# Optimization experiments

Hardware: AMD Instinct MI355X
Metric: run time of the kernel (lower is better)

## Reference

```python
import jax, jax.numpy as jnp
import numpy as np

N_NODES = 10000


def _add_self_loops(edge_index, n):
    loops = jnp.arange(n, dtype=edge_index.dtype)
    row = jnp.concatenate([edge_index[0], loops])
    col = jnp.concatenate([edge_index[1], loops])
    return row, col


def _gcn_norm(row, col, n):
    # symmetric normalization: deg^-1/2[row] * deg^-1/2[col], deg counted on col
    deg = jax.ops.segment_sum(jnp.ones_like(col, dtype=jnp.float32), col, num_segments=n)
    dis = jnp.where(deg > 0, jax.lax.rsqrt(jnp.maximum(deg, 1.0)), 0.0)
    return dis[row] * dis[col]


def _gcn_conv(x, W, b, row, col, norm, n):
    h = x @ W                      # [N, out]
    m = h[row] * norm[:, None]     # [E+N, out] gathered, normalized messages
    out = jax.ops.segment_sum(m, col, num_segments=n)
    return out + b


def setup_inputs() -> dict:
    key = jax.random.key(0)
    ks = jax.random.split(key, 10)
    N, E, Cin, Cout = N_NODES, 160000, 256, 512
    x = jax.random.normal(ks[0], (N, Cin), dtype=jnp.float32)
    edge_index = jax.random.randint(ks[1], (2, E), 0, N, dtype=jnp.int64)
    s = 1.0 / np.sqrt(Cin)
    s2 = 1.0 / np.sqrt(Cout)
    return {
        "x": x,
        "edge_index": edge_index,
        "W1": jax.random.normal(ks[2], (Cin, Cout), dtype=jnp.float32) * s,
        "b1": jnp.zeros((Cout,), dtype=jnp.float32),
        "W2": jax.random.normal(ks[3], (Cout, Cout), dtype=jnp.float32) * s2,
        "b2": jnp.zeros((Cout,), dtype=jnp.float32),
        "W3": jax.random.normal(ks[4], (Cout, Cout), dtype=jnp.float32) * s2,
        "b3": jnp.zeros((Cout,), dtype=jnp.float32),
        "W4": jax.random.normal(ks[5], (Cout, Cout), dtype=jnp.float32) * s2,
        "b4": jnp.zeros((Cout,), dtype=jnp.float32),
    }


def reference(x, edge_index, W1, b1, W2, b2, W3, b3, W4, b4):
    n = x.shape[0]
    row, col = _add_self_loops(edge_index, n)
    norm = _gcn_norm(row, col, n)
    h = jax.nn.relu(_gcn_conv(x, W1, b1, row, col, norm, n))
    h = jax.nn.relu(_gcn_conv(h, W2, b2, row, col, norm, n))
    h = jax.nn.relu(_gcn_conv(h, W3, b3, row, col, norm, n))
    h = _gcn_conv(h, W4, b4, row, col, norm, n)
    return h.reshape(-1, 5, h.shape[-1])  # [N/5, 5, 512]
```

## Files before the change

kernel.cpp:

```cpp
#include <hip/hip_runtime.h>
#include <hip/hip_bf16.h>

#define N_NODES 10000
#define N_EDGES 160000

typedef __hip_bfloat16 bf16;
typedef unsigned short u16;
typedef float f32x4 __attribute__((ext_vector_type(4)));
typedef short s16x8 __attribute__((ext_vector_type(8)));
typedef unsigned short us8 __attribute__((ext_vector_type(8)));
typedef unsigned short us4 __attribute__((ext_vector_type(4)));

static __device__ __forceinline__ float b2f(u16 u) {
    unsigned v = (unsigned)u << 16;
    return __uint_as_float(v);
}
static __device__ __forceinline__ u16 f2b(float f) {
    bf16 b = __float2bfloat16(f);
    return *reinterpret_cast<u16*>(&b);
}

#define GLDS(gp, lp)                                                         \
    __builtin_amdgcn_global_load_lds(                                        \
        (const __attribute__((address_space(1))) void*)(const void*)(gp),    \
        (__attribute__((address_space(3))) void*)(lp), 16, 0, 0)


__global__ void k_prep0(const int* __restrict__ ei,
                        int* __restrict__ row, int* __restrict__ col,
                        int* __restrict__ deg) {
    bool is64 = true;
#pragma unroll
    for (int i = 0; i < 8; ++i) is64 = is64 && (ei[2 * i + 1] == 0);
    int t = blockIdx.x * 256 + threadIdx.x;
    if (t < N_NODES) deg[t] = 0;
    if (t < N_EDGES) {
        if (is64) {
            row[t] = ei[2 * t];
            col[t] = ei[2 * (N_EDGES + t)];
        } else {
            row[t] = ei[t];
            col[t] = ei[N_EDGES + t];
        }
    }
}

__global__ void k_count(const int* __restrict__ col, int* deg) {
    int e = blockIdx.x * 256 + threadIdx.x;
    if (e < N_EDGES) atomicAdd(&deg[col[e]], 1);
}

__global__ void k_scan_all(const int* __restrict__ deg, float* __restrict__ dis,
                           int* __restrict__ off, int* __restrict__ cur) {
    __shared__ int sums[256];
    int t = threadIdx.x;
    const int seg = (N_NODES + 255) >> 8;
    int lo = t * seg, hi = lo + seg;
    if (lo > N_NODES) lo = N_NODES;
    if (hi > N_NODES) hi = N_NODES;
    int s = 0;
    for (int i = lo; i < hi; ++i) {
        dis[i] = rsqrtf((float)deg[i] + 1.0f);
        s += deg[i];
    }
    sums[t] = s;
    __syncthreads();
    for (int d = 1; d < 256; d <<= 1) {
        int v = (t >= d) ? sums[t - d] : 0;
        __syncthreads();
        sums[t] += v;
        __syncthreads();
    }
    int run = sums[t] - s;
    for (int i = lo; i < hi; ++i) {
        off[i] = run;
        cur[i] = run;
        run += deg[i];
    }
    if (t == 255) off[N_NODES] = sums[255];
}

__global__ void k_fill(const int* __restrict__ row, const int* __restrict__ col,
                       const float* __restrict__ dis, int* cur,
                       int* __restrict__ crow, float* __restrict__ cnorm) {
    int e = blockIdx.x * 256 + threadIdx.x;
    if (e < N_EDGES) {
        int r = row[e], c = col[e];
        int p = atomicAdd(&cur[c], 1);
        crow[p] = r;
        cnorm[p] = dis[r] * dis[c];
    }
}


__global__ void k_convx(const float* __restrict__ x, u16* __restrict__ xb) {
    int i = blockIdx.x * 256 + threadIdx.x;
    float4 v = *(const float4*)(x + (size_t)i * 4);
    us4 st;
    st[0] = f2b(v.x); st[1] = f2b(v.y); st[2] = f2b(v.z); st[3] = f2b(v.w);
    *(us4*)(xb + (size_t)i * 4) = st;
}


__global__ void k_transpose(const float* __restrict__ W1, const float* __restrict__ W2,
                            const float* __restrict__ W3, const float* __restrict__ W4,
                            u16* __restrict__ T1, u16* __restrict__ T2,
                            u16* __restrict__ T3, u16* __restrict__ T4) {
    __shared__ u16 tile[32][33];
    int z = blockIdx.z;
    const float* W = (z == 0) ? W1 : (z == 1) ? W2 : (z == 2) ? W3 : W4;
    u16* WT        = (z == 0) ? T1 : (z == 1) ? T2 : (z == 2) ? T3 : T4;
    int K = (z == 0) ? 256 : 512;
    int k0 = blockIdx.y * 32;
    if (k0 >= K) return;
    int n0 = blockIdx.x * 32;
    int tx = threadIdx.x, ty = threadIdx.y;
    for (int i = 0; i < 32; i += 8)
        tile[ty + i][tx] = f2b(W[(size_t)(k0 + ty + i) * 512 + n0 + tx]);
    __syncthreads();
    for (int i = 0; i < 32; i += 8)
        WT[(size_t)(n0 + ty + i) * K + k0 + tx] = tile[tx][ty + i];
}


template <int CE> struct VecT;
template <> struct VecT<4> { typedef us4 T; };
template <> struct VecT<8> { typedef us8 T; };

template <int CE>
__global__ void k_agg(const u16* __restrict__ in, u16* __restrict__ out,
                      const int* __restrict__ off, const int* __restrict__ crow,
                      const float* __restrict__ cnorm, const float* __restrict__ dis) {
    typedef typename VecT<CE>::T VT;
    const int C = CE * 64;
    int node = blockIdx.x * 4 + (threadIdx.x >> 6);
    int lane = threadIdx.x & 63;
    if (node >= N_NODES) return;
    int c = lane * CE;

    float d = dis[node];
    VT sv = *(const VT*)(in + (size_t)node * C + c);
    float acc[CE], acc2[CE];
#pragma unroll
    for (int j = 0; j < CE; ++j) { acc[j] = b2f(sv[j]) * d * d; acc2[j] = 0.f; }

    int b = off[node], e = off[node + 1];
    int i = b;
    for (; i + 1 < e; i += 2) {
        int r0 = crow[i], r1 = crow[i + 1];
        float n0 = cnorm[i], n1 = cnorm[i + 1];
        VT v0 = *(const VT*)(in + (size_t)r0 * C + c);
        VT v1 = *(const VT*)(in + (size_t)r1 * C + c);
#pragma unroll
        for (int j = 0; j < CE; ++j) {
            acc[j]  = fmaf(b2f(v0[j]), n0, acc[j]);
            acc2[j] = fmaf(b2f(v1[j]), n1, acc2[j]);
        }
    }
    if (i < e) {
        int r0 = crow[i];
        float n0 = cnorm[i];
        VT v0 = *(const VT*)(in + (size_t)r0 * C + c);
#pragma unroll
        for (int j = 0; j < CE; ++j) acc[j] = fmaf(b2f(v0[j]), n0, acc[j]);
    }
    VT st;
#pragma unroll
    for (int j = 0; j < CE; ++j) st[j] = f2b(acc[j] + acc2[j]);
    *(VT*)(out + (size_t)node * C + c) = st;
}


static __device__ __forceinline__ void st_out(float* out, size_t idx, float v) { out[idx] = v; }
static __device__ __forceinline__ void st_out(u16* out, size_t idx, float v) { out[idx] = f2b(v); }

template <typename OT>
__global__ __launch_bounds__(256) void k_gemm(
        const u16* __restrict__ A, const u16* __restrict__ BT,
        const float* __restrict__ bias, OT* __restrict__ out,
        int M, int K, int NO, int relu) {
    __shared__ u16 As[2][64][32];
    __shared__ u16 Bs[2][64][32];

    int tid = threadIdx.x;
    int w = tid >> 6;
    int lane = tid & 63;
    int wm = w >> 1, wn = w & 1;
    int m0 = blockIdx.x * 64;
    int n0 = blockIdx.y * 64;
    int l15 = lane & 15;
    int kq = lane >> 4;

    int sp  = w & 1;
    int srb = (w >> 1) * 32;
    int srow = lane >> 2;
    int skc  = (lane & 3) * 8;

    int ar0 = m0 + srb + srow;      if (ar0 > M - 1) ar0 = M - 1;
    int ar1 = m0 + srb + 16 + srow; if (ar1 > M - 1) ar1 = M - 1;
    int br0 = n0 + srb + srow;
    int br1 = br0 + 16;
    const u16* agp0 = A + (size_t)ar0 * K + sp * 32 + skc;
    const u16* agp1 = A + (size_t)ar1 * K + sp * 32 + skc;
    const u16* bgp0 = BT + (size_t)br0 * K + sp * 32 + skc;
    const u16* bgp1 = BT + (size_t)br1 * K + sp * 32 + skc;
    u16* al0 = &As[sp][srb][0];
    u16* al1 = &As[sp][srb + 16][0];
    u16* bl0 = &Bs[sp][srb][0];
    u16* bl1 = &Bs[sp][srb + 16][0];

    int aRow0 = wm * 32 + l15, aRow1 = aRow0 + 16;
    int bRow0 = wn * 32 + l15, bRow1 = bRow0 + 16;

    f32x4 acc00 = {0.f, 0.f, 0.f, 0.f};
    f32x4 acc01 = acc00, acc10 = acc00, acc11 = acc00;

    for (int k0 = 0; k0 < K; k0 += 64) {
        GLDS(agp0 + k0, al0);
        GLDS(agp1 + k0, al1);
        GLDS(bgp0 + k0, bl0);
        GLDS(bgp1 + k0, bl1);
        __syncthreads();
#pragma unroll
        for (int p = 0; p < 2; ++p) {
            s16x8 a0 = *(const s16x8*)&As[p][aRow0][kq * 8];
            s16x8 a1 = *(const s16x8*)&As[p][aRow1][kq * 8];
            s16x8 b0 = *(const s16x8*)&Bs[p][bRow0][kq * 8];
            s16x8 b1 = *(const s16x8*)&Bs[p][bRow1][kq * 8];
            acc00 = __builtin_amdgcn_mfma_f32_16x16x32_bf16(a0, b0, acc00, 0, 0, 0);
            acc01 = __builtin_amdgcn_mfma_f32_16x16x32_bf16(a0, b1, acc01, 0, 0, 0);
            acc10 = __builtin_amdgcn_mfma_f32_16x16x32_bf16(a1, b0, acc10, 0, 0, 0);
            acc11 = __builtin_amdgcn_mfma_f32_16x16x32_bf16(a1, b1, acc11, 0, 0, 0);
        }
        __syncthreads();
    }

    int r0 = (lane >> 4) * 4;
    int cm0 = m0 + wm * 32;
    int cn0 = n0 + wn * 32;
    float bv0 = bias[cn0 + l15];
    float bv1 = bias[cn0 + 16 + l15];
#pragma unroll
    for (int r = 0; r < 4; ++r) {
        int rowa = cm0 + r0 + r;
        if (rowa < M) {
            float v = acc00[r] + bv0;
            if (relu) v = fmaxf(v, 0.f);
            st_out(out, (size_t)rowa * NO + cn0 + l15, v);
            v = acc01[r] + bv1;
            if (relu) v = fmaxf(v, 0.f);
            st_out(out, (size_t)rowa * NO + cn0 + 16 + l15, v);
        }
        int rowb = rowa + 16;
        if (rowb < M) {
            float v = acc10[r] + bv0;
            if (relu) v = fmaxf(v, 0.f);
            st_out(out, (size_t)rowb * NO + cn0 + l15, v);
            v = acc11[r] + bv1;
            if (relu) v = fmaxf(v, 0.f);
            st_out(out, (size_t)rowb * NO + cn0 + 16 + l15, v);
        }
    }
}


extern "C" void kernel_launch(void* const* d_in, const int* in_sizes, int n_in,
                              void* d_out, int out_size, void* d_ws, size_t ws_size,
                              hipStream_t stream) {
    const float* x  = (const float*)d_in[0];
    const int*   ei = (const int*)d_in[1];
    const float* W1 = (const float*)d_in[2];
    const float* b1 = (const float*)d_in[3];
    const float* W2 = (const float*)d_in[4];
    const float* b2 = (const float*)d_in[5];
    const float* W3 = (const float*)d_in[6];
    const float* b3 = (const float*)d_in[7];
    const float* W4 = (const float*)d_in[8];
    const float* b4 = (const float*)d_in[9];

    char* ws = (char*)d_ws;
    size_t o = 0;
    auto alloc = [&](size_t bytes) {
        char* p = ws + o;
        o = (o + bytes + 255) & ~(size_t)255;
        return p;
    };
    int*   row   = (int*)alloc(N_EDGES * 4);
    int*   col   = (int*)alloc(N_EDGES * 4);
    int*   deg   = (int*)alloc(N_NODES * 4);
    float* dis   = (float*)alloc(N_NODES * 4);
    int*   off   = (int*)alloc((N_NODES + 1) * 4);
    int*   cur   = (int*)alloc(N_NODES * 4);
    int*   crow  = (int*)alloc(N_EDGES * 4);
    float* cnorm = (float*)alloc(N_EDGES * 4);
    u16*   WT1   = (u16*)alloc((size_t)512 * 256 * 2);
    u16*   WT2   = (u16*)alloc((size_t)512 * 512 * 2);
    u16*   WT3   = (u16*)alloc((size_t)512 * 512 * 2);
    u16*   WT4   = (u16*)alloc((size_t)512 * 512 * 2);
    u16*   xb    = (u16*)alloc((size_t)N_NODES * 256 * 2);
    u16*   s     = (u16*)alloc((size_t)N_NODES * 512 * 2);
    u16*   h     = (u16*)alloc((size_t)N_NODES * 512 * 2);
    float* outb  = (float*)d_out;

    dim3 b256(256);
    const int gE = (N_EDGES + 255) / 256;
    const dim3 gG(157, 8);
    const int gA = (N_NODES + 3) / 4;

    k_prep0<<<gE, b256, 0, stream>>>(ei, row, col, deg);
    k_count<<<gE, b256, 0, stream>>>(col, deg);
    k_scan_all<<<1, b256, 0, stream>>>(deg, dis, off, cur);
    k_fill<<<gE, b256, 0, stream>>>(row, col, dis, cur, crow, cnorm);
    k_convx<<<N_NODES * 256 / 4 / 256, b256, 0, stream>>>(x, xb);
    k_transpose<<<dim3(16, 16, 4), dim3(32, 8), 0, stream>>>(W1, W2, W3, W4,
                                                             WT1, WT2, WT3, WT4);

    k_agg<4><<<gA, b256, 0, stream>>>(xb, s, off, crow, cnorm, dis);
    k_gemm<u16><<<gG, b256, 0, stream>>>(s, WT1, b1, h, N_NODES, 256, 512, 1);
    k_agg<8><<<gA, b256, 0, stream>>>(h, s, off, crow, cnorm, dis);
    k_gemm<u16><<<gG, b256, 0, stream>>>(s, WT2, b2, h, N_NODES, 512, 512, 1);
    k_agg<8><<<gA, b256, 0, stream>>>(h, s, off, crow, cnorm, dis);
    k_gemm<u16><<<gG, b256, 0, stream>>>(s, WT3, b3, h, N_NODES, 512, 512, 1);
    k_agg<8><<<gA, b256, 0, stream>>>(h, s, off, crow, cnorm, dis);
    k_gemm<float><<<gG, b256, 0, stream>>>(s, WT4, b4, outb, N_NODES, 512, 512, 0);
}
```

Measured before the change: 295.9 us.

## Enlarge GEMM tiles to 128x128 with double buffering, fuse prep kernels, unroll aggregation

The GEMM moves from 64x64 to 128x128 block tiles, with each wave computing a 4x4 grid of MFMA outputs. Global-to-LDS loads are double-buffered so the next K tile loads while the current one is computed. The preprocessing kernels are merged: x conversion, edge unpacking and degree counting now run in one kernel, and CSR fill runs together with the weight transposes. The scan now stages degrees in shared memory, and aggregation unrolls over 4 edges with 4 accumulators. The tradeoffs are more registers and LDS per GEMM block and far fewer GEMM blocks (316), which may underfill the GPU's CUs.

```diff
diff --git a/kernel.cpp b/kernel.cpp
--- a/kernel.cpp
+++ b/kernel.cpp
@@ -26,43 +26,51 @@
         (__attribute__((address_space(3))) void*)(lp), 16, 0, 0)
 
 
-__global__ void k_prep0(const int* __restrict__ ei,
-                        int* __restrict__ row, int* __restrict__ col,
-                        int* __restrict__ deg) {
-    bool is64 = true;
-#pragma unroll
-    for (int i = 0; i < 8; ++i) is64 = is64 && (ei[2 * i + 1] == 0);
+__global__ void k_prep(const int* __restrict__ ei, const float* __restrict__ x,
+                       u16* __restrict__ xb,
+                       int* __restrict__ row, int* __restrict__ col,
+                       int* __restrict__ deg) {
     int t = blockIdx.x * 256 + threadIdx.x;
-    if (t < N_NODES) deg[t] = 0;
+    float4 v = *(const float4*)(x + (size_t)t * 4);
+    us4 st;
+    st[0] = f2b(v.x); st[1] = f2b(v.y); st[2] = f2b(v.z); st[3] = f2b(v.w);
+    *(us4*)(xb + (size_t)t * 4) = st;
+
     if (t < N_EDGES) {
+        bool is64 = true;
+#pragma unroll
+        for (int k = 0; k < 8; ++k) is64 = is64 && (ei[2 * k + 1] == 0);
+        int r, c;
         if (is64) {
-            row[t] = ei[2 * t];
-            col[t] = ei[2 * (N_EDGES + t)];
+            r = ei[2 * t];
+            c = ei[2 * (N_EDGES + t)];
         } else {
-            row[t] = ei[t];
-            col[t] = ei[N_EDGES + t];
+            r = ei[t];
+            c = ei[N_EDGES + t];
         }
-    }
-}
-
-__global__ void k_count(const int* __restrict__ col, int* deg) {
-    int e = blockIdx.x * 256 + threadIdx.x;
-    if (e < N_EDGES) atomicAdd(&deg[col[e]], 1);
+        row[t] = r;
+        col[t] = c;
+        atomicAdd(&deg[c], 1);
+    }
 }
 
 __global__ void k_scan_all(const int* __restrict__ deg, float* __restrict__ dis,
                            int* __restrict__ off, int* __restrict__ cur) {
+    __shared__ int sd[N_NODES];
     __shared__ int sums[256];
     int t = threadIdx.x;
+    for (int i = t; i < N_NODES; i += 256) {
+        int d = deg[i];
+        sd[i] = d;
+        dis[i] = rsqrtf((float)d + 1.0f);
+    }
+    __syncthreads();
     const int seg = (N_NODES + 255) >> 8;
     int lo = t * seg, hi = lo + seg;
     if (lo > N_NODES) lo = N_NODES;
     if (hi > N_NODES) hi = N_NODES;
     int s = 0;
-    for (int i = lo; i < hi; ++i) {
-        dis[i] = rsqrtf((float)deg[i] + 1.0f);
-        s += deg[i];
-    }
+    for (int i = lo; i < hi; ++i) s += sd[i];
     sums[t] = s;
     __syncthreads();
     for (int d = 1; d < 256; d <<= 1) {
@@ -75,46 +83,41 @@
     for (int i = lo; i < hi; ++i) {
         off[i] = run;
         cur[i] = run;
-        run += deg[i];
+        run += sd[i];
     }
     if (t == 255) off[N_NODES] = sums[255];
 }
 
-__global__ void k_fill(const int* __restrict__ row, const int* __restrict__ col,
-                       const float* __restrict__ dis, int* cur,
-                       int* __restrict__ crow, float* __restrict__ cnorm) {
-    int e = blockIdx.x * 256 + threadIdx.x;
-    if (e < N_EDGES) {
-        int r = row[e], c = col[e];
-        int p = atomicAdd(&cur[c], 1);
-        crow[p] = r;
-        cnorm[p] = dis[r] * dis[c];
-    }
-}
-
-
-__global__ void k_convx(const float* __restrict__ x, u16* __restrict__ xb) {
-    int i = blockIdx.x * 256 + threadIdx.x;
-    float4 v = *(const float4*)(x + (size_t)i * 4);
-    us4 st;
-    st[0] = f2b(v.x); st[1] = f2b(v.y); st[2] = f2b(v.z); st[3] = f2b(v.w);
-    *(us4*)(xb + (size_t)i * 4) = st;
-}
-
-
-__global__ void k_transpose(const float* __restrict__ W1, const float* __restrict__ W2,
-                            const float* __restrict__ W3, const float* __restrict__ W4,
-                            u16* __restrict__ T1, u16* __restrict__ T2,
-                            u16* __restrict__ T3, u16* __restrict__ T4) {
+
+__global__ void k_fill_t(const int* __restrict__ row, const int* __restrict__ col,
+                         const float* __restrict__ dis, int* cur,
+                         int* __restrict__ crow, float* __restrict__ cnorm,
+                         const float* __restrict__ W1, const float* __restrict__ W2,
+                         const float* __restrict__ W3, const float* __restrict__ W4,
+                         u16* __restrict__ T1, u16* __restrict__ T2,
+                         u16* __restrict__ T3, u16* __restrict__ T4) {
     __shared__ u16 tile[32][33];
-    int z = blockIdx.z;
+    if (blockIdx.x < 625) {
+        int e = blockIdx.x * 256 + threadIdx.x;
+        if (e < N_EDGES) {
+            int r = row[e], c = col[e];
+            int p = atomicAdd(&cur[c], 1);
+            crow[p] = r;
+            cnorm[p] = dis[r] * dis[c];
+        }
+        return;
+    }
+    int b = blockIdx.x - 625;
+    int z = b >> 8;
+    int rem = b & 255;
+    int by = rem >> 4, bx = rem & 15;
     const float* W = (z == 0) ? W1 : (z == 1) ? W2 : (z == 2) ? W3 : W4;
     u16* WT        = (z == 0) ? T1 : (z == 1) ? T2 : (z == 2) ? T3 : T4;
     int K = (z == 0) ? 256 : 512;
-    int k0 = blockIdx.y * 32;
+    int k0 = by * 32;
     if (k0 >= K) return;
-    int n0 = blockIdx.x * 32;
-    int tx = threadIdx.x, ty = threadIdx.y;
+    int n0 = bx * 32;
+    int tx = threadIdx.x & 31, ty = threadIdx.x >> 5;
     for (int i = 0; i < 32; i += 8)
         tile[ty + i][tx] = f2b(W[(size_t)(k0 + ty + i) * 512 + n0 + tx]);
     __syncthreads();
@@ -135,38 +138,44 @@
     const int C = CE * 64;
     int node = blockIdx.x * 4 + (threadIdx.x >> 6);
     int lane = threadIdx.x & 63;
-    if (node >= N_NODES) return;
     int c = lane * CE;
 
     float d = dis[node];
     VT sv = *(const VT*)(in + (size_t)node * C + c);
-    float acc[CE], acc2[CE];
-#pragma unroll
-    for (int j = 0; j < CE; ++j) { acc[j] = b2f(sv[j]) * d * d; acc2[j] = 0.f; }
+    float a0[CE], a1[CE], a2[CE], a3[CE];
+#pragma unroll
+    for (int j = 0; j < CE; ++j) {
+        a0[j] = b2f(sv[j]) * d * d;
+        a1[j] = 0.f; a2[j] = 0.f; a3[j] = 0.f;
+    }
 
     int b = off[node], e = off[node + 1];
     int i = b;
-    for (; i + 1 < e; i += 2) {
-        int r0 = crow[i], r1 = crow[i + 1];
-        float n0 = cnorm[i], n1 = cnorm[i + 1];
+    for (; i + 3 < e; i += 4) {
+        int r0 = crow[i], r1 = crow[i + 1], r2 = crow[i + 2], r3 = crow[i + 3];
+        float n0 = cnorm[i], n1 = cnorm[i + 1], n2 = cnorm[i + 2], n3 = cnorm[i + 3];
         VT v0 = *(const VT*)(in + (size_t)r0 * C + c);
         VT v1 = *(const VT*)(in + (size_t)r1 * C + c);
+        VT v2 = *(const VT*)(in + (size_t)r2 * C + c);
+        VT v3 = *(const VT*)(in + (size_t)r3 * C + c);
 #pragma unroll
         for (int j = 0; j < CE; ++j) {
-            acc[j]  = fmaf(b2f(v0[j]), n0, acc[j]);
-            acc2[j] = fmaf(b2f(v1[j]), n1, acc2[j]);
+            a0[j] = fmaf(b2f(v0[j]), n0, a0[j]);
+            a1[j] = fmaf(b2f(v1[j]), n1, a1[j]);
+            a2[j] = fmaf(b2f(v2[j]), n2, a2[j]);
+            a3[j] = fmaf(b2f(v3[j]), n3, a3[j]);
         }
     }
-    if (i < e) {
+    for (; i < e; ++i) {
         int r0 = crow[i];
         float n0 = cnorm[i];
         VT v0 = *(const VT*)(in + (size_t)r0 * C + c);
 #pragma unroll
-        for (int j = 0; j < CE; ++j) acc[j] = fmaf(b2f(v0[j]), n0, acc[j]);
+        for (int j = 0; j < CE; ++j) a0[j] = fmaf(b2f(v0[j]), n0, a0[j]);
     }
     VT st;
 #pragma unroll
-    for (int j = 0; j < CE; ++j) st[j] = f2b(acc[j] + acc2[j]);
+    for (int j = 0; j < CE; ++j) st[j] = f2b((a0[j] + a1[j]) + (a2[j] + a3[j]));
     *(VT*)(out + (size_t)node * C + c) = st;
 }
 
@@ -174,91 +183,113 @@
 static __device__ __forceinline__ void st_out(float* out, size_t idx, float v) { out[idx] = v; }
 static __device__ __forceinline__ void st_out(u16* out, size_t idx, float v) { out[idx] = f2b(v); }
 
+static __device__ __forceinline__ void gemm_stage(
+        u16 (*Asb)[128][32], u16 (*Bsb)[128][32],
+        const u16* const aG[4], const u16* const bG[4],
+        const int aP[4], const int aR[4],
+        const int bP[4], const int bR[4], int kk) {
+#pragma unroll
+    for (int q = 0; q < 4; ++q) GLDS(aG[q] + kk, &Asb[aP[q]][aR[q]][0]);
+#pragma unroll
+    for (int q = 0; q < 4; ++q) GLDS(bG[q] + kk, &Bsb[bP[q]][bR[q]][0]);
+}
+
+static __device__ __forceinline__ void gemm_compute(
+        const u16 (*Asb)[128][32], const u16 (*Bsb)[128][32],
+        int wm, int wn, int l15, int kq, f32x4 acc[4][4]) {
+#pragma unroll
+    for (int p = 0; p < 2; ++p) {
+        s16x8 a[4], bb[4];
+#pragma unroll
+        for (int mi = 0; mi < 4; ++mi)
+            a[mi] = *(const s16x8*)&Asb[p][wm * 64 + mi * 16 + l15][kq * 8];
+#pragma unroll
+        for (int ni = 0; ni < 4; ++ni)
+            bb[ni] = *(const s16x8*)&Bsb[p][wn * 64 + ni * 16 + l15][kq * 8];
+#pragma unroll
+        for (int mi = 0; mi < 4; ++mi)
+#pragma unroll
+            for (int ni = 0; ni < 4; ++ni)
+                acc[mi][ni] = __builtin_amdgcn_mfma_f32_16x16x32_bf16(
+                    a[mi], bb[ni], acc[mi][ni], 0, 0, 0);
+    }
+}
+
 template <typename OT>
-__global__ __launch_bounds__(256) void k_gemm(
+__global__ __launch_bounds__(256, 2) void k_gemm(
         const u16* __restrict__ A, const u16* __restrict__ BT,
         const float* __restrict__ bias, OT* __restrict__ out,
         int M, int K, int NO, int relu) {
-    __shared__ u16 As[2][64][32];
-    __shared__ u16 Bs[2][64][32];
+    __shared__ u16 As[2][2][128][32];
+    __shared__ u16 Bs[2][2][128][32];
 
     int tid = threadIdx.x;
     int w = tid >> 6;
     int lane = tid & 63;
     int wm = w >> 1, wn = w & 1;
-    int m0 = blockIdx.x * 64;
-    int n0 = blockIdx.y * 64;
+    int m0 = blockIdx.x * 128;
+    int n0 = blockIdx.y * 128;
     int l15 = lane & 15;
     int kq = lane >> 4;
 
-    int sp  = w & 1;
-    int srb = (w >> 1) * 32;
     int srow = lane >> 2;
-    int skc  = (lane & 3) * 8;
-
-    int ar0 = m0 + srb + srow;      if (ar0 > M - 1) ar0 = M - 1;
-    int ar1 = m0 + srb + 16 + srow; if (ar1 > M - 1) ar1 = M - 1;
-    int br0 = n0 + srb + srow;
-    int br1 = br0 + 16;
-    const u16* agp0 = A + (size_t)ar0 * K + sp * 32 + skc;
-    const u16* agp1 = A + (size_t)ar1 * K + sp * 32 + skc;
-    const u16* bgp0 = BT + (size_t)br0 * K + sp * 32 + skc;
-    const u16* bgp1 = BT + (size_t)br1 * K + sp * 32 + skc;
-    u16* al0 = &As[sp][srb][0];
-    u16* al1 = &As[sp][srb + 16][0];
-    u16* bl0 = &Bs[sp][srb][0];
-    u16* bl1 = &Bs[sp][srb + 16][0];
-
-    int aRow0 = wm * 32 + l15, aRow1 = aRow0 + 16;
-    int bRow0 = wn * 32 + l15, bRow1 = bRow0 + 16;
-
-    f32x4 acc00 = {0.f, 0.f, 0.f, 0.f};
-    f32x4 acc01 = acc00, acc10 = acc00, acc11 = acc00;
-
-    for (int k0 = 0; k0 < K; k0 += 64) {
-        GLDS(agp0 + k0, al0);
-        GLDS(agp1 + k0, al1);
-        GLDS(bgp0 + k0, bl0);
-        GLDS(bgp1 + k0, bl1);
+    int skc = (lane & 3) * 8;
+
+    const u16* aG[4]; const u16* bG[4];
+    int aP[4], aR[4], bP[4], bR[4];
+#pragma unroll
+    for (int q = 0; q < 4; ++q) {
+        int ca = w * 4 + q;
+        aP[q] = ca >> 3;
+        aR[q] = (ca & 7) * 16;
+        int ar = m0 + aR[q] + srow;
+        if (ar > M - 1) ar = M - 1;
+        aG[q] = A + (size_t)ar * K + aP[q] * 32 + skc;
+        int cb = w * 4 + q;
+        bP[q] = cb >> 3;
+        bR[q] = (cb & 7) * 16;
+        int br = n0 + bR[q] + srow;
+        bG[q] = BT + (size_t)br * K + bP[q] * 32 + skc;
+    }
+
+    f32x4 acc[4][4];
+#pragma unroll
+    for (int mi = 0; mi < 4; ++mi)
+#pragma unroll
+        for (int ni = 0; ni < 4; ++ni) acc[mi][ni] = (f32x4){0.f, 0.f, 0.f, 0.f};
+
+    int NT = K >> 6;
+    gemm_stage(As[0], Bs[0], aG, bG, aP, aR, bP, bR, 0);
+    __syncthreads();
+    for (int t = 0; t < NT; t += 2) {
+        gemm_stage(As[1], Bs[1], aG, bG, aP, aR, bP, bR, (t + 1) * 64);
+        gemm_compute(As[0], Bs[0], wm, wn, l15, kq, acc);
         __syncthreads();
-#pragma unroll
-        for (int p = 0; p < 2; ++p) {
-            s16x8 a0 = *(const s16x8*)&As[p][aRow0][kq * 8];
-            s16x8 a1 = *(const s16x8*)&As[p][aRow1][kq * 8];
-            s16x8 b0 = *(const s16x8*)&Bs[p][bRow0][kq * 8];
-            s16x8 b1 = *(const s16x8*)&Bs[p][bRow1][kq * 8];
-            acc00 = __builtin_amdgcn_mfma_f32_16x16x32_bf16(a0, b0, acc00, 0, 0, 0);
-            acc01 = __builtin_amdgcn_mfma_f32_16x16x32_bf16(a0, b1, acc01, 0, 0, 0);
-            acc10 = __builtin_amdgcn_mfma_f32_16x16x32_bf16(a1, b0, acc10, 0, 0, 0);
-            acc11 = __builtin_amdgcn_mfma_f32_16x16x32_bf16(a1, b1, acc11, 0, 0, 0);
-        }
+        if (t + 2 < NT)
+            gemm_stage(As[0], Bs[0], aG, bG, aP, aR, bP, bR, (t + 2) * 64);
+        gemm_compute(As[1], Bs[1], wm, wn, l15, kq, acc);
         __syncthreads();
     }
 
-    int r0 = (lane >> 4) * 4;
-    int cm0 = m0 + wm * 32;
-    int cn0 = n0 + wn * 32;
-    float bv0 = bias[cn0 + l15];
-    float bv1 = bias[cn0 + 16 + l15];
-#pragma unroll
-    for (int r = 0; r < 4; ++r) {
-        int rowa = cm0 + r0 + r;
-        if (rowa < M) {
-            float v = acc00[r] + bv0;
-            if (relu) v = fmaxf(v, 0.f);
-            st_out(out, (size_t)rowa * NO + cn0 + l15, v);
-            v = acc01[r] + bv1;
-            if (relu) v = fmaxf(v, 0.f);
-            st_out(out, (size_t)rowa * NO + cn0 + 16 + l15, v);
-        }
-        int rowb = rowa + 16;
-        if (rowb < M) {
-            float v = acc10[r] + bv0;
-            if (relu) v = fmaxf(v, 0.f);
-            st_out(out, (size_t)rowb * NO + cn0 + l15, v);
-            v = acc11[r] + bv1;
-            if (relu) v = fmaxf(v, 0.f);
-            st_out(out, (size_t)rowb * NO + cn0 + 16 + l15, v);
+    int r0o = (lane >> 4) * 4;
+    int cm = m0 + wm * 64;
+    int cn = n0 + wn * 64;
+    float bv[4];
+#pragma unroll
+    for (int ni = 0; ni < 4; ++ni) bv[ni] = bias[cn + ni * 16 + l15];
+#pragma unroll
+    for (int mi = 0; mi < 4; ++mi) {
+#pragma unroll
+        for (int r = 0; r < 4; ++r) {
+            int rowa = cm + mi * 16 + r0o + r;
+            if (rowa < M) {
+#pragma unroll
+                for (int ni = 0; ni < 4; ++ni) {
+                    float v = acc[mi][ni][r] + bv[ni];
+                    if (relu) v = fmaxf(v, 0.f);
+                    st_out(out, (size_t)rowa * NO + cn + ni * 16 + l15, v);
+                }
+            }
         }
     }
 }
@@ -303,17 +334,15 @@
     float* outb  = (float*)d_out;
 
     dim3 b256(256);
-    const int gE = (N_EDGES + 255) / 256;
-    const dim3 gG(157, 8);
-    const int gA = (N_NODES + 3) / 4;
-
-    k_prep0<<<gE, b256, 0, stream>>>(ei, row, col, deg);
-    k_count<<<gE, b256, 0, stream>>>(col, deg);
+    const dim3 gG(79, 4);
+    const int  gA = (N_NODES + 3) / 4;
+    const int  gP = N_NODES * 256 / 4 / 256;
+
+    hipMemsetAsync(deg, 0, N_NODES * 4, stream);
+    k_prep<<<gP, b256, 0, stream>>>(ei, x, xb, row, col, deg);
     k_scan_all<<<1, b256, 0, stream>>>(deg, dis, off, cur);
-    k_fill<<<gE, b256, 0, stream>>>(row, col, dis, cur, crow, cnorm);
-    k_convx<<<N_NODES * 256 / 4 / 256, b256, 0, stream>>>(x, xb);
-    k_transpose<<<dim3(16, 16, 4), dim3(32, 8), 0, stream>>>(W1, W2, W3, W4,
-                                                             WT1, WT2, WT3, WT4);
+    k_fill_t<<<625 + 1024, b256, 0, stream>>>(row, col, dis, cur, crow, cnorm,
+                                              W1, W2, W3, W4, WT1, WT2, WT3, WT4);
 
     k_agg<4><<<gA, b256, 0, stream>>>(xb, s, off, crow, cnorm, dis);
     k_gemm<u16><<<gG, b256, 0, stream>>>(s, WT1, b1, h, N_NODES, 256, 512, 1);
```

New measurement: 274.4 us. 1.08x faster.
